# Performance work log

Hardware: AMD Instinct MI355X
Metric: run time of the kernel (lower is better)

Reference implementation:

```python
import jax, jax.numpy as jnp
import numpy as np
from jax import lax

B, C, H, W = 16, 256, 56, 56
MID = 16  # SE: max(C//16, 4)
EPS = 1e-5


def _bn(x, g, b, m, v):
    # inference-mode BatchNorm2d folded to per-channel scale/shift
    s = g * lax.rsqrt(v + EPS)
    return x * s[None, :, None, None] + (b - m * s)[None, :, None, None]


def _dw(x, w, ph, pw):
    # depthwise conv, NCHW, kernel w: [C,1,kh,kw]
    return lax.conv_general_dilated(
        x, w, window_strides=(1, 1), padding=[(ph, ph), (pw, pw)],
        dimension_numbers=('NCHW', 'OIHW', 'NCHW'), feature_group_count=C)


def _pw(x, w):
    # 1x1 conv, w: [O,C,1,1]
    return jnp.einsum('bchw,oc->bohw', x, w[:, :, 0, 0])


def _se(x, w1, b1, w2, b2):
    s = x.mean(axis=(2, 3))                      # [B,C] squeeze
    s = jax.nn.relu(s @ w1.T + b1)               # [B,MID]
    s = jax.nn.sigmoid(s @ w2.T + b2)            # [B,C]
    return x * s[:, :, None, None]


def setup_inputs() -> dict:
    key = jax.random.key(0)
    ks = jax.random.split(key, 32)
    rn = lambda i, shape, sc=0.05: jax.random.normal(ks[i], shape, jnp.float32) * sc
    ru = lambda i, shape: jax.random.uniform(ks[i], shape, jnp.float32)
    return {
        'x': rn(0, (B, C, H, W), 1.0),
        'pw1_w': rn(1, (C, C, 1, 1)),
        'xy3_w': rn(2, (C, 1, 3, 3)), 'xy5_w': rn(3, (C, 1, 5, 5)),
        'bnxy_g': ru(4, (C,)), 'bnxy_b': rn(5, (C,)), 'bnxy_m': rn(6, (C,)), 'bnxy_v': ru(7, (C,)),
        'xz3_w': rn(8, (C, 1, 1, 3)), 'xz5_w': rn(9, (C, 1, 1, 5)),
        'bnxz_g': ru(10, (C,)), 'bnxz_b': rn(11, (C,)), 'bnxz_m': rn(12, (C,)), 'bnxz_v': ru(13, (C,)),
        'yz3_w': rn(14, (C, 1, 3, 1)), 'yz5_w': rn(15, (C, 1, 5, 1)),
        'bnyz_g': ru(16, (C,)), 'bnyz_b': rn(17, (C,)), 'bnyz_m': rn(18, (C,)), 'bnyz_v': ru(19, (C,)),
        'alpha': jnp.full((1, C, 1, 1), 0.5, jnp.float32),
        'beta': jnp.full((1, C, 1, 1), 0.5, jnp.float32),
        'pw2_w': rn(20, (C, C, 1, 1)),
        'bn2_g': ru(21, (C,)), 'bn2_b': rn(22, (C,)), 'bn2_m': rn(23, (C,)), 'bn2_v': ru(24, (C,)),
        'fc1_w': rn(25, (MID, C)), 'fc1_b': rn(26, (MID,)),
        'fc2_w': rn(27, (C, MID)), 'fc2_b': rn(28, (C,)),
    }


def reference(x, pw1_w, xy3_w, xy5_w, bnxy_g, bnxy_b, bnxy_m, bnxy_v,
              xz3_w, xz5_w, bnxz_g, bnxz_b, bnxz_m, bnxz_v,
              yz3_w, yz5_w, bnyz_g, bnyz_b, bnyz_m, bnyz_v,
              alpha, beta, pw2_w, bn2_g, bn2_b, bn2_m, bn2_v,
              fc1_w, fc1_b, fc2_w, fc2_b):
    # Pw1: 1x1 conv, no BN / no act
    out = _pw(x, pw1_w)
    # MS_TOP (stride=1 -> pool is identity)
    # [B] xy branch: DW 3x3 + DW 5x5 -> BN -> ReLU
    f_xy = jax.nn.relu(_bn(_dw(out, xy3_w, 1, 1) + _dw(out, xy5_w, 2, 2),
                           bnxy_g, bnxy_b, bnxy_m, bnxy_v))
    # [A] xz branch: per-row depthwise Conv1d along W == depthwise (1,k) 2D conv
    f_xz = jax.nn.relu(_bn(_dw(out, xz3_w, 0, 1) + _dw(out, xz5_w, 0, 2),
                           bnxz_g, bnxz_b, bnxz_m, bnxz_v))
    # [A] yz branch: per-column depthwise Conv1d along H == depthwise (k,1) 2D conv
    f_yz = jax.nn.relu(_bn(_dw(out, yz3_w, 1, 0) + _dw(out, yz5_w, 2, 0),
                           bnyz_g, bnyz_b, bnyz_m, bnyz_v))
    # [C] learnable-gate fusion
    gate = jax.nn.sigmoid(alpha * f_xz + beta * f_yz)
    top = jax.nn.relu(f_xy * gate)
    # Pw2: 1x1 conv -> BN -> ReLU
    out2 = jax.nn.relu(_bn(_pw(top, pw2_w), bn2_g, bn2_b, bn2_m, bn2_v))
    # SE channel attention
    out2 = _se(out2, fc1_w, fc1_b, fc2_w, fc2_b)
    # DropPath is identity at inference; shortcut is identity (stride=1, in==out)
    return out2 + x
```

## Files before the change

### kernel.cpp

```cpp
#include <hip/hip_runtime.h>
#include <math.h>

typedef __bf16 bf16;
typedef __bf16 bf16x8 __attribute__((ext_vector_type(8)));
typedef __bf16 bf16x4 __attribute__((ext_vector_type(4)));
typedef float f32x4 __attribute__((ext_vector_type(4)));

#define CC 256
#define BB 16
#define HH 56
#define WW 56
#define HWSZ 3136
#define EPS 1e-5f

#define OFF_SCALE 0
#define OFF_SUMS  16384
#define OFF_WBF1  32768
#define OFF_WBF2  163840
#define OFF_WDW   294912
#define OFF_BNC   312832
#define OFF_OUT2  321024

__device__ __forceinline__ f32x4 cvt4(bf16x4 v) {
    union { bf16x4 b; unsigned int u[2]; } q; q.b = v;
    f32x4 r;
    r[0] = __uint_as_float(q.u[0] << 16);
    r[1] = __uint_as_float(q.u[0] & 0xffff0000u);
    r[2] = __uint_as_float(q.u[1] << 16);
    r[3] = __uint_as_float(q.u[1] & 0xffff0000u);
    return r;
}

__global__ __launch_bounds__(256) void precast(
    const float* __restrict__ w1, const float* __restrict__ w2,
    const float* __restrict__ xy3, const float* __restrict__ xy5,
    const float* __restrict__ xz3, const float* __restrict__ xz5,
    const float* __restrict__ yz3, const float* __restrict__ yz5,
    const float* __restrict__ gxy, const float* __restrict__ bxy,
    const float* __restrict__ mxy, const float* __restrict__ vxy,
    const float* __restrict__ gxz, const float* __restrict__ bxz,
    const float* __restrict__ mxz, const float* __restrict__ vxz,
    const float* __restrict__ gyz, const float* __restrict__ byz,
    const float* __restrict__ myz, const float* __restrict__ vyz,
    const float* __restrict__ alpha, const float* __restrict__ beta,
    bf16* __restrict__ wbf1, bf16* __restrict__ wbf2,
    bf16* __restrict__ wdw, float* __restrict__ bnc,
    float* __restrict__ sums)
{
    const int blk = blockIdx.x, t = threadIdx.x;
    if (blk < 128) {
        int i = blk * 512 + t * 2;
        wbf1[i] = (bf16)w1[i]; wbf1[i + 1] = (bf16)w1[i + 1];
    } else if (blk < 256) {
        int i = (blk - 128) * 512 + t * 2;
        wbf2[i] = (bf16)w2[i]; wbf2[i + 1] = (bf16)w2[i + 1];
    } else {
        const int c = t;
#pragma unroll
        for (int dh = 0; dh < 5; ++dh)
#pragma unroll
            for (int dw = 0; dw < 5; ++dw) {
                float v = xy5[c * 25 + dh * 5 + dw];
                if (dh >= 1 && dh <= 3 && dw >= 1 && dw <= 3)
                    v += xy3[c * 9 + (dh - 1) * 3 + (dw - 1)];
                wdw[(dh * 5 + dw) * CC + c] = (bf16)v;
            }
#pragma unroll
        for (int d = 0; d < 5; ++d) {
            float v = xz5[c * 5 + d];
            if (d >= 1 && d <= 3) v += xz3[c * 3 + d - 1];
            wdw[(25 + d) * CC + c] = (bf16)v;
            float u = yz5[c * 5 + d];
            if (d >= 1 && d <= 3) u += yz3[c * 3 + d - 1];
            wdw[(30 + d) * CC + c] = (bf16)u;
        }
        float s;
        s = gxy[c] * rsqrtf(vxy[c] + EPS); bnc[0*CC+c] = s; bnc[1*CC+c] = bxy[c] - mxy[c]*s;
        s = gxz[c] * rsqrtf(vxz[c] + EPS); bnc[2*CC+c] = s; bnc[3*CC+c] = bxz[c] - mxz[c]*s;
        s = gyz[c] * rsqrtf(vyz[c] + EPS); bnc[4*CC+c] = s; bnc[5*CC+c] = byz[c] - myz[c]*s;
        bnc[6*CC+c] = alpha[c]; bnc[7*CC+c] = beta[c];
        for (int i = t; i < BB * CC; i += 256) sums[i] = 0.f;
    }
}

__global__ __launch_bounds__(256, 3) void pw_gemm1(
    const float* __restrict__ in, const bf16* __restrict__ wbf,
    bf16* __restrict__ mid)
{
    __shared__ __align__(16) bf16 XT[64][264];
    const int hw0 = blockIdx.x * 64;
    const int b   = blockIdx.y;
    const int t   = threadIdx.x;
    const int lane = t & 63, wv = t >> 6;
    const int q = lane >> 4, n = lane & 15;
    const int co_w = wv * 64;

    bf16x8 aq[4][4];
    const bf16* wp[4];
#pragma unroll
    for (int cf = 0; cf < 4; ++cf) {
        wp[cf] = wbf + (size_t)(co_w + cf * 16 + n) * CC + q * 8;
#pragma unroll
        for (int kx = 0; kx < 4; ++kx)
            aq[cf][kx] = *(const bf16x8*)(wp[cf] + kx * 32);
    }

    {
        const int hwg = (t & 15) * 4;
        const int cig = (t >> 4) * 4;
        const float* base = in + (size_t)b * CC * HWSZ + hw0 + hwg;
#pragma unroll
        for (int pass = 0; pass < 4; ++pass) {
            const int ci0 = pass * 64 + cig;
            f32x4 v[4];
#pragma unroll
            for (int i = 0; i < 4; ++i)
                v[i] = *(const f32x4*)(base + (size_t)(ci0 + i) * HWSZ);
#pragma unroll
            for (int j = 0; j < 4; ++j) {
                bf16x4 r = {(bf16)v[0][j], (bf16)v[1][j], (bf16)v[2][j], (bf16)v[3][j]};
                *(bf16x4*)(&XT[hwg + j][ci0]) = r;
            }
        }
    }
    __syncthreads();

    f32x4 acc[4][4] = {};
#pragma unroll
    for (int half = 0; half < 2; ++half) {
#pragma unroll
        for (int kx = 0; kx < 4; ++kx) {
            const int kk = half * 4 + kx;
            bf16x8 bq[4];
#pragma unroll
            for (int hf = 0; hf < 4; ++hf)
                bq[hf] = *(const bf16x8*)(&XT[hf * 16 + n][kk * 32 + q * 8]);
#pragma unroll
            for (int cf = 0; cf < 4; ++cf)
#pragma unroll
                for (int hf = 0; hf < 4; ++hf)
                    acc[cf][hf] = __builtin_amdgcn_mfma_f32_16x16x32_bf16(
                        aq[cf][kx], bq[hf], acc[cf][hf], 0, 0, 0);
        }
        if (half == 0) {
#pragma unroll
            for (int cf = 0; cf < 4; ++cf)
#pragma unroll
                for (int kx = 0; kx < 4; ++kx)
                    aq[cf][kx] = *(const bf16x8*)(wp[cf] + 128 + kx * 32);
        }
    }

    bf16* ob = mid + ((size_t)b * HWSZ + hw0) * CC;
#pragma unroll
    for (int cf = 0; cf < 4; ++cf) {
        const int co4 = co_w + cf * 16 + q * 4;
#pragma unroll
        for (int hf = 0; hf < 4; ++hf) {
            bf16x4 r = {(bf16)acc[cf][hf][0], (bf16)acc[cf][hf][1],
                        (bf16)acc[cf][hf][2], (bf16)acc[cf][hf][3]};
            *(bf16x4*)(ob + (size_t)(hf * 16 + n) * CC + co4) = r;
        }
    }
}

__global__ __launch_bounds__(256) void dwfuse(
    const bf16* __restrict__ mid, const bf16* __restrict__ wdw,
    const float* __restrict__ bnc, bf16* __restrict__ top)
{
    __shared__ __align__(16) bf16 lw[35 * 256];
    const int t = threadIdx.x;
#pragma unroll
    for (int i = 0; i < 4; ++i)
        *(bf16x8*)(&lw[(i * 256 + t) * 8]) = *(const bf16x8*)(wdw + (i * 256 + t) * 8);
    if (t < 96)
        *(bf16x8*)(&lw[(1024 + t) * 8]) = *(const bf16x8*)(wdw + (1024 + t) * 8);
    __syncthreads();

    const int lane = t & 63;
    const int wb = blockIdx.x * 8 + (t >> 6) * 2;
    const int h0 = blockIdx.y * 2;
    const size_t plane = (size_t)blockIdx.z * HWSZ;
    const int c0 = lane * 4;

    f32x4 axy[2][2] = {}, axz[2][2] = {}, ayz[2][2] = {};

#pragma unroll
    for (int dhh = 0; dhh < 6; ++dhh) {
        const int hh = h0 - 2 + dhh;
        if ((unsigned)hh >= (unsigned)HH) continue;
        const bf16* rowp = mid + (plane + (size_t)hh * WW) * CC + c0;

        f32x4 fv[6];
#pragma unroll
        for (int wc = 0; wc < 6; ++wc) {
            const int ww = wb - 2 + wc;
            f32x4 f = {0.f, 0.f, 0.f, 0.f};
            if ((unsigned)ww < (unsigned)WW)
                f = cvt4(*(const bf16x4*)(rowp + (size_t)ww * CC));
            fv[wc] = f;
        }

#pragma unroll
        for (int ph = 0; ph < 2; ++ph) {
            const int dh = dhh - ph;
            if (dh < 0 || dh > 4) continue;
#pragma unroll
            for (int dw = 0; dw < 5; ++dw) {
                const f32x4 wt = cvt4(*(const bf16x4*)(&lw[(dh * 5 + dw) * CC + c0]));
                axy[ph][0] += wt * fv[dw];
                axy[ph][1] += wt * fv[dw + 1];
            }
            if (dh == 2) {
#pragma unroll
                for (int dw = 0; dw < 5; ++dw) {
                    const f32x4 wt = cvt4(*(const bf16x4*)(&lw[(25 + dw) * CC + c0]));
                    axz[ph][0] += wt * fv[dw];
                    axz[ph][1] += wt * fv[dw + 1];
                }
            }
            {
                const f32x4 wt = cvt4(*(const bf16x4*)(&lw[(30 + dh) * CC + c0]));
                ayz[ph][0] += wt * fv[2];
                ayz[ph][1] += wt * fv[3];
            }
        }
    }

    const f32x4 sxy = *(const f32x4*)(bnc + 0 * CC + c0);
    const f32x4 hxy = *(const f32x4*)(bnc + 1 * CC + c0);
    const f32x4 sxz = *(const f32x4*)(bnc + 2 * CC + c0);
    const f32x4 hxz = *(const f32x4*)(bnc + 3 * CC + c0);
    const f32x4 syz = *(const f32x4*)(bnc + 4 * CC + c0);
    const f32x4 hyz = *(const f32x4*)(bnc + 5 * CC + c0);
    const f32x4 al  = *(const f32x4*)(bnc + 6 * CC + c0);
    const f32x4 be  = *(const f32x4*)(bnc + 7 * CC + c0);

#pragma unroll
    for (int ph = 0; ph < 2; ++ph)
#pragma unroll
        for (int pw = 0; pw < 2; ++pw) {
            const f32x4 txy = axy[ph][pw] * sxy + hxy;
            const f32x4 txz = axz[ph][pw] * sxz + hxz;
            const f32x4 tyz = ayz[ph][pw] * syz + hyz;
            bf16x4 r;
#pragma unroll
            for (int j = 0; j < 4; ++j) {
                const float fxy = fmaxf(txy[j], 0.f);
                const float fxz = fmaxf(txz[j], 0.f);
                const float fyz = fmaxf(tyz[j], 0.f);
                const float z   = al[j] * fxz + be[j] * fyz;
                const float g   = 1.f / (1.f + __expf(-z));
                r[j] = (bf16)(fxy * g);
            }
            *(bf16x4*)(top + (plane + (size_t)(h0 + ph) * WW + (wb + pw)) * CC + c0) = r;
        }
}

__global__ __launch_bounds__(256, 3) void pw_gemm2(
    const bf16* __restrict__ top, const bf16* __restrict__ wbf,
    const float* __restrict__ g2, const float* __restrict__ b2,
    const float* __restrict__ m2, const float* __restrict__ v2,
    bf16* __restrict__ out2, float* __restrict__ sums)
{
    __shared__ __align__(16) bf16 XT[64][264];
    const int hw0 = blockIdx.x * 64;
    const int b   = blockIdx.y;
    const int t   = threadIdx.x;
    const int lane = t & 63, wv = t >> 6;
    const int q = lane >> 4, n = lane & 15;
    const int co_w = wv * 64;

    bf16x8 aq[4][4];
    const bf16* wp[4];
#pragma unroll
    for (int cf = 0; cf < 4; ++cf) {
        wp[cf] = wbf + (size_t)(co_w + cf * 16 + n) * CC + q * 8;
#pragma unroll
        for (int kx = 0; kx < 4; ++kx)
            aq[cf][kx] = *(const bf16x8*)(wp[cf] + kx * 32);
    }

    {
        const int hw_r = t >> 2;
        const int k0   = (t & 3) * 64;
        const bf16* src = top + ((size_t)b * HWSZ + hw0 + hw_r) * CC + k0;
#pragma unroll
        for (int j = 0; j < 8; ++j)
            *(bf16x8*)(&XT[hw_r][k0 + j * 8]) = *(const bf16x8*)(src + j * 8);
    }
    __syncthreads();

    f32x4 acc[4][4] = {};
#pragma unroll
    for (int half = 0; half < 2; ++half) {
#pragma unroll
        for (int kx = 0; kx < 4; ++kx) {
            const int kk = half * 4 + kx;
            bf16x8 bq[4];
#pragma unroll
            for (int hf = 0; hf < 4; ++hf)
                bq[hf] = *(const bf16x8*)(&XT[hf * 16 + n][kk * 32 + q * 8]);
#pragma unroll
            for (int cf = 0; cf < 4; ++cf)
#pragma unroll
                for (int hf = 0; hf < 4; ++hf)
                    acc[cf][hf] = __builtin_amdgcn_mfma_f32_16x16x32_bf16(
                        aq[cf][kx], bq[hf], acc[cf][hf], 0, 0, 0);
        }
        if (half == 0) {
#pragma unroll
            for (int cf = 0; cf < 4; ++cf)
#pragma unroll
                for (int kx = 0; kx < 4; ++kx)
                    aq[cf][kx] = *(const bf16x8*)(wp[cf] + 128 + kx * 32);
        }
    }

    bf16* ob = out2 + ((size_t)b * HWSZ + hw0) * CC;
#pragma unroll
    for (int cf = 0; cf < 4; ++cf) {
        const int co4 = co_w + cf * 16 + q * 4;
        f32x4 g = *(const f32x4*)(g2 + co4);
        f32x4 bb = *(const f32x4*)(b2 + co4);
        f32x4 mm = *(const f32x4*)(m2 + co4);
        f32x4 vv = *(const f32x4*)(v2 + co4);
        f32x4 sc, sh;
#pragma unroll
        for (int r = 0; r < 4; ++r) {
            sc[r] = g[r] * rsqrtf(vv[r] + EPS);
            sh[r] = bb[r] - mm[r] * sc[r];
        }
        f32x4 rs = {};
#pragma unroll
        for (int hf = 0; hf < 4; ++hf) {
            bf16x4 r4;
#pragma unroll
            for (int r = 0; r < 4; ++r) {
                float v = fmaxf(acc[cf][hf][r] * sc[r] + sh[r], 0.f);
                rs[r] += v;
                r4[r] = (bf16)v;
            }
            *(bf16x4*)(ob + (size_t)(hf * 16 + n) * CC + co4) = r4;
        }
#pragma unroll
        for (int msk = 1; msk < 16; msk <<= 1)
#pragma unroll
            for (int r = 0; r < 4; ++r) rs[r] += __shfl_xor(rs[r], msk);
        if (n == 0) {
#pragma unroll
            for (int r = 0; r < 4; ++r)
                atomicAdd(&sums[b * CC + co4 + r], rs[r]);
        }
    }
}

__global__ __launch_bounds__(256) void se_fc(
    const float* __restrict__ sums,
    const float* __restrict__ w1, const float* __restrict__ b1,
    const float* __restrict__ w2, const float* __restrict__ b2,
    float* __restrict__ scale)
{
    __shared__ float mean[256];
    __shared__ float hid[16];
    const int b = blockIdx.x, tid = threadIdx.x;
    mean[tid] = sums[b * CC + tid] * (1.f / (float)HWSZ);
    __syncthreads();
    if (tid < 16) {
        float h = b1[tid];
        for (int cd = 0; cd < 256; ++cd) h += w1[tid * 256 + cd] * mean[cd];
        hid[tid] = fmaxf(h, 0.f);
    }
    __syncthreads();
    float v = b2[tid];
#pragma unroll
    for (int md = 0; md < 16; ++md) v += w2[tid * 16 + md] * hid[md];
    scale[b * CC + tid] = 1.f / (1.f + expf(-v));
}

__global__ __launch_bounds__(256) void se_apply(
    const bf16* __restrict__ out2, const float* __restrict__ x,
    const float* __restrict__ scale, float* __restrict__ out)
{
    __shared__ float TT[64 * 68];
    const int hw0 = blockIdx.x * 64;
    const int c0  = blockIdx.y * 64;
    const int b   = blockIdx.z;
    const int t   = threadIdx.x;

    {
        const int hw_r = t >> 2;
        const int coff = (t & 3) * 16;
        const bf16* p = out2 + ((size_t)b * HWSZ + hw0 + hw_r) * CC + c0 + coff;
        bf16x8 u0 = *(const bf16x8*)(p);
        bf16x8 u1 = *(const bf16x8*)(p + 8);
        const float* sp = scale + b * CC + c0 + coff;
        f32x4 s0 = *(const f32x4*)(sp), s1 = *(const f32x4*)(sp + 4);
        f32x4 s2 = *(const f32x4*)(sp + 8), s3 = *(const f32x4*)(sp + 12);
#pragma unroll
        for (int j = 0; j < 4; ++j) {
            TT[(coff + j)      * 68 + hw_r] = (float)u0[j]     * s0[j];
            TT[(coff + 4 + j)  * 68 + hw_r] = (float)u0[4 + j] * s1[j];
            TT[(coff + 8 + j)  * 68 + hw_r] = (float)u1[j]     * s2[j];
            TT[(coff + 12 + j) * 68 + hw_r] = (float)u1[4 + j] * s3[j];
        }
    }
    __syncthreads();
    {
        const int c_r   = t >> 2;
        const int hwoff = (t & 3) * 16;
        const size_t go = ((size_t)b * CC + c0 + c_r) * HWSZ + hw0 + hwoff;
#pragma unroll
        for (int v = 0; v < 4; ++v) {
            f32x4 tv = *(const f32x4*)(&TT[c_r * 68 + hwoff + v * 4]);
            f32x4 xv = *(const f32x4*)(x + go + v * 4);
#pragma unroll
            for (int j = 0; j < 4; ++j) tv[j] += xv[j];
            *(f32x4*)(out + go + v * 4) = tv;
        }
    }
}

extern "C" void kernel_launch(void* const* d_in, const int* in_sizes, int n_in,
                              void* d_out, int out_size, void* d_ws, size_t ws_size,
                              hipStream_t stream)
{
    const float* x      = (const float*)d_in[0];
    const float* pw1_w  = (const float*)d_in[1];
    const float* xy3_w  = (const float*)d_in[2];
    const float* xy5_w  = (const float*)d_in[3];
    const float* bnxy_g = (const float*)d_in[4];
    const float* bnxy_b = (const float*)d_in[5];
    const float* bnxy_m = (const float*)d_in[6];
    const float* bnxy_v = (const float*)d_in[7];
    const float* xz3_w  = (const float*)d_in[8];
    const float* xz5_w  = (const float*)d_in[9];
    const float* bnxz_g = (const float*)d_in[10];
    const float* bnxz_b = (const float*)d_in[11];
    const float* bnxz_m = (const float*)d_in[12];
    const float* bnxz_v = (const float*)d_in[13];
    const float* yz3_w  = (const float*)d_in[14];
    const float* yz5_w  = (const float*)d_in[15];
    const float* bnyz_g = (const float*)d_in[16];
    const float* bnyz_b = (const float*)d_in[17];
    const float* bnyz_m = (const float*)d_in[18];
    const float* bnyz_v = (const float*)d_in[19];
    const float* alpha  = (const float*)d_in[20];
    const float* beta   = (const float*)d_in[21];
    const float* pw2_w  = (const float*)d_in[22];
    const float* bn2_g  = (const float*)d_in[23];
    const float* bn2_b  = (const float*)d_in[24];
    const float* bn2_m  = (const float*)d_in[25];
    const float* bn2_v  = (const float*)d_in[26];
    const float* fc1_w  = (const float*)d_in[27];
    const float* fc1_b  = (const float*)d_in[28];
    const float* fc2_w  = (const float*)d_in[29];
    const float* fc2_b  = (const float*)d_in[30];

    const size_t NEL = (size_t)BB * CC * HWSZ;
    char* ws = (char*)d_ws;
    float* scale = (float*)(ws + OFF_SCALE);
    float* sums  = (float*)(ws + OFF_SUMS);
    bf16*  wbf1  = (bf16*) (ws + OFF_WBF1);
    bf16*  wbf2  = (bf16*) (ws + OFF_WBF2);
    bf16*  wdw   = (bf16*) (ws + OFF_WDW);
    float* bnc   = (float*)(ws + OFF_BNC);
    bf16*  out2  = (bf16*) (ws + OFF_OUT2);
    bf16*  mid   = (bf16*)d_out;
    bf16*  top   = (bf16*)d_out + NEL;

    precast<<<257, 256, 0, stream>>>(pw1_w, pw2_w,
        xy3_w, xy5_w, xz3_w, xz5_w, yz3_w, yz5_w,
        bnxy_g, bnxy_b, bnxy_m, bnxy_v,
        bnxz_g, bnxz_b, bnxz_m, bnxz_v,
        bnyz_g, bnyz_b, bnyz_m, bnyz_v,
        alpha, beta, wbf1, wbf2, wdw, bnc, sums);

    pw_gemm1<<<dim3(49, 16), 256, 0, stream>>>(x, wbf1, mid);
    dwfuse<<<dim3(7, 28, 16), 256, 0, stream>>>(mid, wdw, bnc, top);
    pw_gemm2<<<dim3(49, 16), 256, 0, stream>>>(top, wbf2, bn2_g, bn2_b,
                                               bn2_m, bn2_v, out2, sums);
    se_fc<<<BB, 256, 0, stream>>>(sums, fc1_w, fc1_b, fc2_w, fc2_b, scale);
    se_apply<<<dim3(49, 4, 16), 256, 0, stream>>>(out2, x, scale, (float*)d_out);
}
```

Measured before the change: 291.9 us.

## Widen depthwise tile, double-buffer rows, fp32 LDS weights; fuse SE FC into apply

The depthwise fusion kernel now computes 4 output columns per thread instead of 2, so each loaded input row is reused across more outputs. Row loads are double-buffered so the next row's global loads overlap the current row's FMAs. Weights are kept as fp32 in shared memory to avoid repeated bf16 conversion. Separately, the SE fully-connected kernel is folded into se_apply, which removes one launch but recomputes the small MLP in every block. The 4x16 grid covers 64 columns, so the extra columns past the edge are masked; register pressure also rises.

```diff
diff --git a/kernel.cpp b/kernel.cpp
--- a/kernel.cpp
+++ b/kernel.cpp
@@ -164,68 +164,92 @@
     }
 }
 
-__global__ __launch_bounds__(256) void dwfuse(
+__global__ __launch_bounds__(256, 2) void dwfuse(
     const bf16* __restrict__ mid, const bf16* __restrict__ wdw,
     const float* __restrict__ bnc, bf16* __restrict__ top)
 {
-    __shared__ __align__(16) bf16 lw[35 * 256];
+    __shared__ __align__(16) float lwf[35 * 256];
     const int t = threadIdx.x;
 #pragma unroll
-    for (int i = 0; i < 4; ++i)
-        *(bf16x8*)(&lw[(i * 256 + t) * 8]) = *(const bf16x8*)(wdw + (i * 256 + t) * 8);
-    if (t < 96)
-        *(bf16x8*)(&lw[(1024 + t) * 8]) = *(const bf16x8*)(wdw + (1024 + t) * 8);
+    for (int k = 0; k < 35; ++k)
+        lwf[k * 256 + t] = (float)wdw[k * 256 + t];
     __syncthreads();
 
     const int lane = t & 63;
-    const int wb = blockIdx.x * 8 + (t >> 6) * 2;
+    const int wb = blockIdx.x * 16 + (t >> 6) * 4;
     const int h0 = blockIdx.y * 2;
     const size_t plane = (size_t)blockIdx.z * HWSZ;
     const int c0 = lane * 4;
-
-    f32x4 axy[2][2] = {}, axz[2][2] = {}, ayz[2][2] = {};
-
-#pragma unroll
-    for (int dhh = 0; dhh < 6; ++dhh) {
-        const int hh = h0 - 2 + dhh;
-        if ((unsigned)hh >= (unsigned)HH) continue;
-        const bf16* rowp = mid + (plane + (size_t)hh * WW) * CC + c0;
-
-        f32x4 fv[6];
-#pragma unroll
-        for (int wc = 0; wc < 6; ++wc) {
-            const int ww = wb - 2 + wc;
-            f32x4 f = {0.f, 0.f, 0.f, 0.f};
-            if ((unsigned)ww < (unsigned)WW)
-                f = cvt4(*(const bf16x4*)(rowp + (size_t)ww * CC));
-            fv[wc] = f;
-        }
-
-#pragma unroll
-        for (int ph = 0; ph < 2; ++ph) {
-            const int dh = dhh - ph;
-            if (dh < 0 || dh > 4) continue;
-#pragma unroll
-            for (int dw = 0; dw < 5; ++dw) {
-                const f32x4 wt = cvt4(*(const bf16x4*)(&lw[(dh * 5 + dw) * CC + c0]));
-                axy[ph][0] += wt * fv[dw];
-                axy[ph][1] += wt * fv[dw + 1];
-            }
-            if (dh == 2) {
-#pragma unroll
-                for (int dw = 0; dw < 5; ++dw) {
-                    const f32x4 wt = cvt4(*(const bf16x4*)(&lw[(25 + dw) * CC + c0]));
-                    axz[ph][0] += wt * fv[dw];
-                    axz[ph][1] += wt * fv[dw + 1];
-                }
-            }
-            {
-                const f32x4 wt = cvt4(*(const bf16x4*)(&lw[(30 + dh) * CC + c0]));
-                ayz[ph][0] += wt * fv[2];
-                ayz[ph][1] += wt * fv[3];
-            }
-        }
-    }
+    const bf16* gbase = mid + plane * CC + c0;
+
+    f32x4 axy[2][4] = {}, axz[2][4] = {}, ayz[2][4] = {};
+    bf16x4 rA[8], rB[8];
+
+#define LOADROW(DHH, BUF) do {                                               \
+    const int hh_ = h0 - 2 + (DHH);                                          \
+    if ((unsigned)hh_ < (unsigned)HH) {                                      \
+        const bf16* rp_ = gbase + (size_t)hh_ * WW * CC;                     \
+        _Pragma("unroll")                                                    \
+        for (int wc_ = 0; wc_ < 8; ++wc_) {                                  \
+            const int ww_ = wb - 2 + wc_;                                    \
+            if ((unsigned)ww_ < (unsigned)WW)                                \
+                BUF[wc_] = *(const bf16x4*)(rp_ + (size_t)ww_ * CC);         \
+            else { bf16x4 z_ = {}; BUF[wc_] = z_; }                          \
+        }                                                                    \
+    } else {                                                                 \
+        _Pragma("unroll")                                                    \
+        for (int wc_ = 0; wc_ < 8; ++wc_) { bf16x4 z_ = {}; BUF[wc_] = z_; } \
+    }                                                                        \
+} while (0)
+
+#define COMPROW(DHH, BUF) do {                                               \
+    f32x4 fv_[8];                                                            \
+    _Pragma("unroll")                                                        \
+    for (int wc_ = 0; wc_ < 8; ++wc_) fv_[wc_] = cvt4(BUF[wc_]);             \
+    _Pragma("unroll")                                                        \
+    for (int ph_ = 0; ph_ < 2; ++ph_) {                                      \
+        const int dh_ = (DHH) - ph_;                                         \
+        if (dh_ < 0 || dh_ > 4) continue;                                    \
+        _Pragma("unroll")                                                    \
+        for (int dw_ = 0; dw_ < 5; ++dw_) {                                  \
+            const f32x4 wt_ = *(const f32x4*)(&lwf[(dh_ * 5 + dw_) * CC + c0]); \
+            _Pragma("unroll")                                                \
+            for (int pw_ = 0; pw_ < 4; ++pw_)                                \
+                axy[ph_][pw_] += wt_ * fv_[dw_ + pw_];                       \
+        }                                                                    \
+        if (dh_ == 2) {                                                      \
+            _Pragma("unroll")                                                \
+            for (int dw_ = 0; dw_ < 5; ++dw_) {                              \
+                const f32x4 wz_ = *(const f32x4*)(&lwf[(25 + dw_) * CC + c0]); \
+                _Pragma("unroll")                                            \
+                for (int pw_ = 0; pw_ < 4; ++pw_)                            \
+                    axz[ph_][pw_] += wz_ * fv_[dw_ + pw_];                   \
+            }                                                                \
+        }                                                                    \
+        {                                                                    \
+            const f32x4 wy_ = *(const f32x4*)(&lwf[(30 + dh_) * CC + c0]);   \
+            _Pragma("unroll")                                                \
+            for (int pw_ = 0; pw_ < 4; ++pw_)                                \
+                ayz[ph_][pw_] += wy_ * fv_[2 + pw_];                         \
+        }                                                                    \
+    }                                                                        \
+} while (0)
+
+    LOADROW(0, rA);
+    LOADROW(1, rB);
+    COMPROW(0, rA);
+    LOADROW(2, rA);
+    COMPROW(1, rB);
+    LOADROW(3, rB);
+    COMPROW(2, rA);
+    LOADROW(4, rA);
+    COMPROW(3, rB);
+    LOADROW(5, rB);
+    COMPROW(4, rA);
+    COMPROW(5, rB);
+
+#undef LOADROW
+#undef COMPROW
 
     const f32x4 sxy = *(const f32x4*)(bnc + 0 * CC + c0);
     const f32x4 hxy = *(const f32x4*)(bnc + 1 * CC + c0);
@@ -239,7 +263,8 @@
 #pragma unroll
     for (int ph = 0; ph < 2; ++ph)
 #pragma unroll
-        for (int pw = 0; pw < 2; ++pw) {
+        for (int pw = 0; pw < 4; ++pw) {
+            const int w = wb + pw;
             const f32x4 txy = axy[ph][pw] * sxy + hxy;
             const f32x4 txz = axz[ph][pw] * sxz + hxz;
             const f32x4 tyz = ayz[ph][pw] * syz + hyz;
@@ -253,7 +278,8 @@
                 const float g   = 1.f / (1.f + __expf(-z));
                 r[j] = (bf16)(fxy * g);
             }
-            *(bf16x4*)(top + (plane + (size_t)(h0 + ph) * WW + (wb + pw)) * CC + c0) = r;
+            if (w < WW)
+                *(bf16x4*)(top + (plane + (size_t)(h0 + ph) * WW + w) * CC + c0) = r;
         }
 }
 
@@ -355,38 +381,44 @@
     }
 }
 
-__global__ __launch_bounds__(256) void se_fc(
+__global__ __launch_bounds__(256) void se_apply(
+    const bf16* __restrict__ out2, const float* __restrict__ x,
     const float* __restrict__ sums,
     const float* __restrict__ w1, const float* __restrict__ b1,
     const float* __restrict__ w2, const float* __restrict__ b2,
-    float* __restrict__ scale)
+    float* __restrict__ out)
 {
+    __shared__ float TT[64 * 68];
     __shared__ float mean[256];
     __shared__ float hid[16];
-    const int b = blockIdx.x, tid = threadIdx.x;
-    mean[tid] = sums[b * CC + tid] * (1.f / (float)HWSZ);
-    __syncthreads();
-    if (tid < 16) {
-        float h = b1[tid];
-        for (int cd = 0; cd < 256; ++cd) h += w1[tid * 256 + cd] * mean[cd];
-        hid[tid] = fmaxf(h, 0.f);
-    }
-    __syncthreads();
-    float v = b2[tid];
-#pragma unroll
-    for (int md = 0; md < 16; ++md) v += w2[tid * 16 + md] * hid[md];
-    scale[b * CC + tid] = 1.f / (1.f + expf(-v));
-}
-
-__global__ __launch_bounds__(256) void se_apply(
-    const bf16* __restrict__ out2, const float* __restrict__ x,
-    const float* __restrict__ scale, float* __restrict__ out)
-{
-    __shared__ float TT[64 * 68];
+    __shared__ __align__(16) float scl[64];
     const int hw0 = blockIdx.x * 64;
     const int c0  = blockIdx.y * 64;
     const int b   = blockIdx.z;
     const int t   = threadIdx.x;
+
+    mean[t] = sums[b * CC + t] * (1.f / (float)HWSZ);
+    __syncthreads();
+    {
+        const int m = t >> 4, l = t & 15;
+        const float* wr = w1 + m * CC + l * 16;
+        const float* mr = mean + l * 16;
+        float h = 0.f;
+#pragma unroll
+        for (int j = 0; j < 16; ++j) h += wr[j] * mr[j];
+#pragma unroll
+        for (int msk = 1; msk < 16; msk <<= 1) h += __shfl_xor(h, msk);
+        if (l == 0) hid[m] = fmaxf(h + b1[m], 0.f);
+    }
+    __syncthreads();
+    if (t < 64) {
+        const int c = c0 + t;
+        float v = b2[c];
+#pragma unroll
+        for (int md = 0; md < 16; ++md) v += w2[c * 16 + md] * hid[md];
+        scl[t] = 1.f / (1.f + __expf(-v));
+    }
+    __syncthreads();
 
     {
         const int hw_r = t >> 2;
@@ -394,9 +426,10 @@
         const bf16* p = out2 + ((size_t)b * HWSZ + hw0 + hw_r) * CC + c0 + coff;
         bf16x8 u0 = *(const bf16x8*)(p);
         bf16x8 u1 = *(const bf16x8*)(p + 8);
-        const float* sp = scale + b * CC + c0 + coff;
-        f32x4 s0 = *(const f32x4*)(sp), s1 = *(const f32x4*)(sp + 4);
-        f32x4 s2 = *(const f32x4*)(sp + 8), s3 = *(const f32x4*)(sp + 12);
+        f32x4 s0 = *(const f32x4*)(&scl[coff]);
+        f32x4 s1 = *(const f32x4*)(&scl[coff + 4]);
+        f32x4 s2 = *(const f32x4*)(&scl[coff + 8]);
+        f32x4 s3 = *(const f32x4*)(&scl[coff + 12]);
 #pragma unroll
         for (int j = 0; j < 4; ++j) {
             TT[(coff + j)      * 68 + hw_r] = (float)u0[j]     * s0[j];
@@ -459,7 +492,6 @@
 
     const size_t NEL = (size_t)BB * CC * HWSZ;
     char* ws = (char*)d_ws;
-    float* scale = (float*)(ws + OFF_SCALE);
     float* sums  = (float*)(ws + OFF_SUMS);
     bf16*  wbf1  = (bf16*) (ws + OFF_WBF1);
     bf16*  wbf2  = (bf16*) (ws + OFF_WBF2);
@@ -477,9 +509,9 @@
         alpha, beta, wbf1, wbf2, wdw, bnc, sums);
 
     pw_gemm1<<<dim3(49, 16), 256, 0, stream>>>(x, wbf1, mid);
-    dwfuse<<<dim3(7, 28, 16), 256, 0, stream>>>(mid, wdw, bnc, top);
+    dwfuse<<<dim3(4, 28, 16), 256, 0, stream>>>(mid, wdw, bnc, top);
     pw_gemm2<<<dim3(49, 16), 256, 0, stream>>>(top, wbf2, bn2_g, bn2_b,
                                                bn2_m, bn2_v, out2, sums);
-    se_fc<<<BB, 256, 0, stream>>>(sums, fc1_w, fc1_b, fc2_w, fc2_b, scale);
-    se_apply<<<dim3(49, 4, 16), 256, 0, stream>>>(out2, x, scale, (float*)d_out);
-}
+    se_apply<<<dim3(49, 4, 16), 256, 0, stream>>>(out2, x, sums,
+        fc1_w, fc1_b, fc2_w, fc2_b, (float*)d_out);
+}
```

New measurement: 603.2 us. +106.6%, slower.

## Fuse SE FC into apply kernel; prefetch dwfuse inputs before fp32 weight staging

Applied to the files above, without the earlier changes.

The dwfuse kernel now issues all 36 bf16 input loads into registers before staging the depthwise weights into shared memory, and it stores those weights as fp32 so the inner loop no longer converts them. It also sets launch bounds to 2 blocks per SM. The se_fc kernel is removed, and every se_apply block recomputes the SE squeeze MLP from the channel sums, which saves one launch. In exchange, the MLP is computed redundantly in every block, and the 36 held loads add register pressure.

```diff
diff --git a/kernel.cpp b/kernel.cpp
--- a/kernel.cpp
+++ b/kernel.cpp
@@ -164,65 +164,69 @@
     }
 }
 
-__global__ __launch_bounds__(256) void dwfuse(
+__global__ __launch_bounds__(256, 2) void dwfuse(
     const bf16* __restrict__ mid, const bf16* __restrict__ wdw,
     const float* __restrict__ bnc, bf16* __restrict__ top)
 {
-    __shared__ __align__(16) bf16 lw[35 * 256];
+    __shared__ __align__(16) float lwf[35 * 256];
     const int t = threadIdx.x;
-#pragma unroll
-    for (int i = 0; i < 4; ++i)
-        *(bf16x8*)(&lw[(i * 256 + t) * 8]) = *(const bf16x8*)(wdw + (i * 256 + t) * 8);
-    if (t < 96)
-        *(bf16x8*)(&lw[(1024 + t) * 8]) = *(const bf16x8*)(wdw + (1024 + t) * 8);
-    __syncthreads();
-
     const int lane = t & 63;
     const int wb = blockIdx.x * 8 + (t >> 6) * 2;
     const int h0 = blockIdx.y * 2;
     const size_t plane = (size_t)blockIdx.z * HWSZ;
     const int c0 = lane * 4;
-
-    f32x4 axy[2][2] = {}, axz[2][2] = {}, ayz[2][2] = {};
-
-#pragma unroll
-    for (int dhh = 0; dhh < 6; ++dhh) {
-        const int hh = h0 - 2 + dhh;
-        if ((unsigned)hh >= (unsigned)HH) continue;
-        const bf16* rowp = mid + (plane + (size_t)hh * WW) * CC + c0;
-
-        f32x4 fv[6];
+    const bf16* gbase = mid + plane * CC + c0;
+
+    bf16x4 raw[6][6];
+#pragma unroll
+    for (int r = 0; r < 6; ++r) {
+        const int hh = h0 - 2 + r;
+        const bool hok = (unsigned)hh < (unsigned)HH;
+        const bf16* rp = gbase + (ptrdiff_t)hh * (WW * CC);
 #pragma unroll
         for (int wc = 0; wc < 6; ++wc) {
             const int ww = wb - 2 + wc;
-            f32x4 f = {0.f, 0.f, 0.f, 0.f};
-            if ((unsigned)ww < (unsigned)WW)
-                f = cvt4(*(const bf16x4*)(rowp + (size_t)ww * CC));
-            fv[wc] = f;
-        }
-
+            bf16x4 v = {};
+            if (hok && (unsigned)ww < (unsigned)WW)
+                v = *(const bf16x4*)(rp + (ptrdiff_t)ww * CC);
+            raw[r][wc] = v;
+        }
+    }
+    __builtin_amdgcn_sched_barrier(0);
+
+#pragma unroll
+    for (int k = 0; k < 35; ++k)
+        lwf[k * 256 + t] = (float)wdw[k * 256 + t];
+    __syncthreads();
+
+    f32x4 axy[2][2] = {}, axz[2][2] = {}, ayz[2][2] = {};
+#pragma unroll
+    for (int r = 0; r < 6; ++r) {
+        f32x4 fv[6];
+#pragma unroll
+        for (int wc = 0; wc < 6; ++wc) fv[wc] = cvt4(raw[r][wc]);
 #pragma unroll
         for (int ph = 0; ph < 2; ++ph) {
-            const int dh = dhh - ph;
+            const int dh = r - ph;
             if (dh < 0 || dh > 4) continue;
 #pragma unroll
             for (int dw = 0; dw < 5; ++dw) {
-                const f32x4 wt = cvt4(*(const bf16x4*)(&lw[(dh * 5 + dw) * CC + c0]));
+                const f32x4 wt = *(const f32x4*)(&lwf[(dh * 5 + dw) * CC + c0]);
                 axy[ph][0] += wt * fv[dw];
                 axy[ph][1] += wt * fv[dw + 1];
             }
             if (dh == 2) {
 #pragma unroll
                 for (int dw = 0; dw < 5; ++dw) {
-                    const f32x4 wt = cvt4(*(const bf16x4*)(&lw[(25 + dw) * CC + c0]));
-                    axz[ph][0] += wt * fv[dw];
-                    axz[ph][1] += wt * fv[dw + 1];
+                    const f32x4 wz = *(const f32x4*)(&lwf[(25 + dw) * CC + c0]);
+                    axz[ph][0] += wz * fv[dw];
+                    axz[ph][1] += wz * fv[dw + 1];
                 }
             }
             {
-                const f32x4 wt = cvt4(*(const bf16x4*)(&lw[(30 + dh) * CC + c0]));
-                ayz[ph][0] += wt * fv[2];
-                ayz[ph][1] += wt * fv[3];
+                const f32x4 wy = *(const f32x4*)(&lwf[(30 + dh) * CC + c0]);
+                ayz[ph][0] += wy * fv[2];
+                ayz[ph][1] += wy * fv[3];
             }
         }
     }
@@ -243,7 +247,7 @@
             const f32x4 txy = axy[ph][pw] * sxy + hxy;
             const f32x4 txz = axz[ph][pw] * sxz + hxz;
             const f32x4 tyz = ayz[ph][pw] * syz + hyz;
-            bf16x4 r;
+            bf16x4 rr;
 #pragma unroll
             for (int j = 0; j < 4; ++j) {
                 const float fxy = fmaxf(txy[j], 0.f);
@@ -251,9 +255,9 @@
                 const float fyz = fmaxf(tyz[j], 0.f);
                 const float z   = al[j] * fxz + be[j] * fyz;
                 const float g   = 1.f / (1.f + __expf(-z));
-                r[j] = (bf16)(fxy * g);
-            }
-            *(bf16x4*)(top + (plane + (size_t)(h0 + ph) * WW + (wb + pw)) * CC + c0) = r;
+                rr[j] = (bf16)(fxy * g);
+            }
+            *(bf16x4*)(top + (plane + (size_t)(h0 + ph) * WW + (wb + pw)) * CC + c0) = rr;
         }
 }
 
@@ -355,38 +359,44 @@
     }
 }
 
-__global__ __launch_bounds__(256) void se_fc(
+__global__ __launch_bounds__(256) void se_apply(
+    const bf16* __restrict__ out2, const float* __restrict__ x,
     const float* __restrict__ sums,
     const float* __restrict__ w1, const float* __restrict__ b1,
     const float* __restrict__ w2, const float* __restrict__ b2,
-    float* __restrict__ scale)
-{
+    float* __restrict__ out)
+{
+    __shared__ float TT[64 * 68];
     __shared__ float mean[256];
     __shared__ float hid[16];
-    const int b = blockIdx.x, tid = threadIdx.x;
-    mean[tid] = sums[b * CC + tid] * (1.f / (float)HWSZ);
-    __syncthreads();
-    if (tid < 16) {
-        float h = b1[tid];
-        for (int cd = 0; cd < 256; ++cd) h += w1[tid * 256 + cd] * mean[cd];
-        hid[tid] = fmaxf(h, 0.f);
-    }
-    __syncthreads();
-    float v = b2[tid];
-#pragma unroll
-    for (int md = 0; md < 16; ++md) v += w2[tid * 16 + md] * hid[md];
-    scale[b * CC + tid] = 1.f / (1.f + expf(-v));
-}
-
-__global__ __launch_bounds__(256) void se_apply(
-    const bf16* __restrict__ out2, const float* __restrict__ x,
-    const float* __restrict__ scale, float* __restrict__ out)
-{
-    __shared__ float TT[64 * 68];
+    __shared__ __align__(16) float scl[64];
     const int hw0 = blockIdx.x * 64;
     const int c0  = blockIdx.y * 64;
     const int b   = blockIdx.z;
     const int t   = threadIdx.x;
+
+    mean[t] = sums[b * CC + t] * (1.f / (float)HWSZ);
+    __syncthreads();
+    {
+        const int m = t >> 4, l = t & 15;
+        const float* wr = w1 + m * CC + l * 16;
+        const float* mr = mean + l * 16;
+        float h = 0.f;
+#pragma unroll
+        for (int j = 0; j < 16; ++j) h += wr[j] * mr[j];
+#pragma unroll
+        for (int msk = 1; msk < 16; msk <<= 1) h += __shfl_xor(h, msk);
+        if (l == 0) hid[m] = fmaxf(h + b1[m], 0.f);
+    }
+    __syncthreads();
+    if (t < 64) {
+        const int c = c0 + t;
+        float v = b2[c];
+#pragma unroll
+        for (int md = 0; md < 16; ++md) v += w2[c * 16 + md] * hid[md];
+        scl[t] = 1.f / (1.f + __expf(-v));
+    }
+    __syncthreads();
 
     {
         const int hw_r = t >> 2;
@@ -394,9 +404,10 @@
         const bf16* p = out2 + ((size_t)b * HWSZ + hw0 + hw_r) * CC + c0 + coff;
         bf16x8 u0 = *(const bf16x8*)(p);
         bf16x8 u1 = *(const bf16x8*)(p + 8);
-        const float* sp = scale + b * CC + c0 + coff;
-        f32x4 s0 = *(const f32x4*)(sp), s1 = *(const f32x4*)(sp + 4);
-        f32x4 s2 = *(const f32x4*)(sp + 8), s3 = *(const f32x4*)(sp + 12);
+        f32x4 s0 = *(const f32x4*)(&scl[coff]);
+        f32x4 s1 = *(const f32x4*)(&scl[coff + 4]);
+        f32x4 s2 = *(const f32x4*)(&scl[coff + 8]);
+        f32x4 s3 = *(const f32x4*)(&scl[coff + 12]);
 #pragma unroll
         for (int j = 0; j < 4; ++j) {
             TT[(coff + j)      * 68 + hw_r] = (float)u0[j]     * s0[j];
@@ -459,7 +470,6 @@
 
     const size_t NEL = (size_t)BB * CC * HWSZ;
     char* ws = (char*)d_ws;
-    float* scale = (float*)(ws + OFF_SCALE);
     float* sums  = (float*)(ws + OFF_SUMS);
     bf16*  wbf1  = (bf16*) (ws + OFF_WBF1);
     bf16*  wbf2  = (bf16*) (ws + OFF_WBF2);
@@ -480,6 +490,6 @@
     dwfuse<<<dim3(7, 28, 16), 256, 0, stream>>>(mid, wdw, bnc, top);
     pw_gemm2<<<dim3(49, 16), 256, 0, stream>>>(top, wbf2, bn2_g, bn2_b,
                                                bn2_m, bn2_v, out2, sums);
-    se_fc<<<BB, 256, 0, stream>>>(sums, fc1_w, fc1_b, fc2_w, fc2_b, scale);
-    se_apply<<<dim3(49, 4, 16), 256, 0, stream>>>(out2, x, scale, (float*)d_out);
-}
+    se_apply<<<dim3(49, 4, 16), 256, 0, stream>>>(out2, x, sums,
+        fc1_w, fc1_b, fc2_w, fc2_b, (float*)d_out);
+}
```

Measured after the change: 262.3 us. 10.1% less time.
